# Kernel tuning notes

Hardware: AMD Instinct MI355X
Metric: run time of the kernel (lower is better)

The kernel has to match this reference:

```python
import jax, jax.numpy as jnp
import numpy as np

N, E, G = 50000, 640000, 1024
D, RD, H = 128, 200, 512
NUM_ATOM_FEATS, ATOM_VOCAB = 9, 64
NUM_BOND_FEATS, BOND_VOCAB = 3, 16


def setup_inputs() -> dict:
    key = jax.random.key(0)
    ks = jax.random.split(key, 24)
    inp = {
        "x_feat": jax.random.randint(ks[0], (N, NUM_ATOM_FEATS), 0, ATOM_VOCAB),
        "edge_index": jax.random.randint(ks[1], (2, E), 0, N),
        "edge_attr_feat": jax.random.randint(ks[2], (E, NUM_BOND_FEATS), 0, BOND_VOCAB),
        "batch": jnp.sort(jax.random.randint(ks[3], (N,), 0, G)),
        "rdkit_feats": jax.random.normal(ks[4], (G, RD), dtype=jnp.float32),
        # learned params
        "atom_emb": jax.random.normal(ks[5], (NUM_ATOM_FEATS, ATOM_VOCAB, D), dtype=jnp.float32) * 0.02,
        "bond_emb": jax.random.normal(ks[6], (NUM_BOND_FEATS, BOND_VOCAB, D), dtype=jnp.float32) * 0.02,
        "conv1_w1": jax.random.normal(ks[7], (D, D), dtype=jnp.float32) / np.sqrt(D),
        "conv1_b1": jnp.zeros((D,), jnp.float32),
        "conv1_w2": jax.random.normal(ks[8], (D, D), dtype=jnp.float32) / np.sqrt(D),
        "conv1_b2": jnp.zeros((D,), jnp.float32),
        "conv2_w1": jax.random.normal(ks[9], (D, D), dtype=jnp.float32) / np.sqrt(D),
        "conv2_b1": jnp.zeros((D,), jnp.float32),
        "conv2_w2": jax.random.normal(ks[10], (D, D), dtype=jnp.float32) / np.sqrt(D),
        "conv2_b2": jnp.zeros((D,), jnp.float32),
        "mlp_w1": jax.random.normal(ks[11], (D + RD, H), dtype=jnp.float32) / np.sqrt(D + RD),
        "mlp_b1": jnp.zeros((H,), jnp.float32),
        "mlp_w2": jax.random.normal(ks[12], (H, H // 2), dtype=jnp.float32) / np.sqrt(H),
        "mlp_b2": jnp.zeros((H // 2,), jnp.float32),
        "mlp_w3": jax.random.normal(ks[13], (H // 2, 1), dtype=jnp.float32) / np.sqrt(H // 2),
        "mlp_b3": jnp.zeros((1,), jnp.float32),
    }
    return inp


def _gine_conv(x, edge_index, edge_attr, w1, b1, w2, b2, eps=0.0):
    # PyG GINEConv: out = nn((1+eps)*x + sum_{j in N(i)} relu(x_j + e_ji))
    src, dst = edge_index[0], edge_index[1]
    msg = jax.nn.relu(x[src] + edge_attr)               # [E, D]
    agg = jax.ops.segment_sum(msg, dst, num_segments=x.shape[0])  # [N, D]
    h = (1.0 + eps) * x + agg
    h = jax.nn.relu(h @ w1 + b1)
    return h @ w2 + b2


def reference(x_feat, edge_index, edge_attr_feat, batch, rdkit_feats,
              atom_emb, bond_emb,
              conv1_w1, conv1_b1, conv1_w2, conv1_b2,
              conv2_w1, conv2_b1, conv2_w2, conv2_b2,
              mlp_w1, mlp_b1, mlp_w2, mlp_b2, mlp_w3, mlp_b3):
    # AtomEncoder / BondEncoder: sum of per-feature categorical embeddings
    x = atom_emb[jnp.arange(NUM_ATOM_FEATS)[None, :], x_feat].sum(axis=1)          # [N, D]
    edge_attr = bond_emb[jnp.arange(NUM_BOND_FEATS)[None, :], edge_attr_feat].sum(axis=1)  # [E, D]

    x = _gine_conv(x, edge_index, edge_attr, conv1_w1, conv1_b1, conv1_w2, conv1_b2)
    x = _gine_conv(x, edge_index, edge_attr, conv2_w1, conv2_b1, conv2_w2, conv2_b2)

    # global mean pool over graphs
    sums = jax.ops.segment_sum(x, batch, num_segments=G)                # [G, D]
    counts = jax.ops.segment_sum(jnp.ones((x.shape[0],), x.dtype), batch, num_segments=G)
    pooled = sums / jnp.maximum(counts, 1.0)[:, None]

    h = jnp.concatenate([pooled, rdkit_feats], axis=1)                  # [G, D+RD]
    h = jax.nn.relu(h @ mlp_w1 + mlp_b1)   # dropout is identity in eval mode
    h = jax.nn.relu(h @ mlp_w2 + mlp_b2)
    return h @ mlp_w3 + mlp_b3                                          # [G, 1]
```

## Files before the change

### kernel.cpp

```cpp
#include <hip/hip_runtime.h>

#define N_NODES 50000
#define N_EDGES 640000
#define N_GRAPH 1024
#define D 128
#define RD 200
#define CAP 64

typedef __attribute__((ext_vector_type(4))) float f32x4;
typedef __attribute__((ext_vector_type(8))) float f32x8;
typedef __attribute__((ext_vector_type(4))) _Float16 half4;
typedef __attribute__((ext_vector_type(8))) _Float16 half8;

__global__ void k_prep(const float* __restrict__ w0, const float* __restrict__ w1,
                       const float* __restrict__ w2, const float* __restrict__ w3,
                       const float* __restrict__ mw1, const float* __restrict__ mw2,
                       const float* __restrict__ emb,
                       _Float16* __restrict__ cWf,
                       _Float16* __restrict__ W1f,
                       _Float16* __restrict__ W2f,
                       _Float16* __restrict__ embh,
                       int* __restrict__ deg) {
  int t = blockIdx.x * 256 + threadIdx.x;
  if (t < N_NODES) deg[t] = 0;
  if (t < 8192) {
    int mat = t >> 11, r = t & 2047;
    int frag = r >> 6, lane = r & 63;
    int n0 = frag >> 2, kk = frag & 3;
    int n = n0 * 16 + (lane & 15);
    int kb = (lane >> 4) * 8 + kk * 32;
    const float* W = (mat == 0) ? w0 : (mat == 1) ? w1 : (mat == 2) ? w2 : w3;
    half8 o;
#pragma unroll
    for (int j = 0; j < 8; ++j) o[j] = (_Float16)W[(kb + j) * D + n];
    *(half8*)&cWf[((size_t)mat * 2048 + r) * 8] = o;
  } else if (t < 8192 + 22528) {
    int u = t - 8192;
    int frag = u >> 6, lane = u & 63;
    int n0 = frag / 11, kk = frag % 11;
    int n = n0 * 16 + (lane & 15);
    int kb = (lane >> 4) * 8 + kk * 32;
    half8 o;
#pragma unroll
    for (int j = 0; j < 8; ++j) {
      int k = kb + j;
      o[j] = (k < 328) ? (_Float16)mw1[k * 512 + n] : (_Float16)0.f;
    }
    *(half8*)&W1f[(size_t)u * 8] = o;
  } else if (t < 8192 + 22528 + 16384) {
    int u = t - 8192 - 22528;
    int frag = u >> 6, lane = u & 63;
    int n0 = frag >> 4, kk = frag & 15;
    int n = n0 * 16 + (lane & 15);
    int kb = (lane >> 4) * 8 + kk * 32;
    half8 o;
#pragma unroll
    for (int j = 0; j < 8; ++j) o[j] = (_Float16)mw2[(kb + j) * 256 + n];
    *(half8*)&W2f[(size_t)u * 8] = o;
  } else if (t < 8192 + 22528 + 16384 + 9216) {
    int u = t - 8192 - 22528 - 16384;
    float4 v0 = *(const float4*)&emb[(size_t)u * 8];
    float4 v1 = *(const float4*)&emb[(size_t)u * 8 + 4];
    half8 o;
    o[0] = (_Float16)v0.x; o[1] = (_Float16)v0.y; o[2] = (_Float16)v0.z; o[3] = (_Float16)v0.w;
    o[4] = (_Float16)v1.x; o[5] = (_Float16)v1.y; o[6] = (_Float16)v1.z; o[7] = (_Float16)v1.w;
    *(half8*)&embh[(size_t)u * 8] = o;
  }
}

__global__ void k_atom_count(const int* __restrict__ xf, const _Float16* __restrict__ embh,
                             _Float16* __restrict__ x16,
                             const int* __restrict__ ei, const int* __restrict__ bondf,
                             const int* __restrict__ batch,
                             int* __restrict__ deg, int* __restrict__ csr1,
                             int* __restrict__ gstart) {
  if (blockIdx.x < 3125) {
    int t = blockIdx.x * 256 + threadIdx.x;
    int node = t >> 4, c = (t & 15) << 3;
    if ((t & 15) == 0) {
      int b = batch[node];
      int prev = (node == 0) ? -1 : batch[node - 1];
      for (int g = prev + 1; g <= b; ++g) gstart[g] = node;
      if (node == N_NODES - 1)
        for (int g = b + 1; g <= N_GRAPH; ++g) gstart[g] = N_NODES;
    }
    int v[9];
#pragma unroll
    for (int f = 0; f < 9; ++f) v[f] = xf[node * 9 + f];
    f32x8 a = (f32x8)(0.f);
#pragma unroll
    for (int f = 0; f < 9; ++f) {
      half8 e8 = *(const half8*)&embh[(size_t)(f * 64 + v[f]) * D + c];
      a += __builtin_convertvector(e8, f32x8);
    }
    half8 o;
#pragma unroll
    for (int tt = 0; tt < 8; ++tt) o[tt] = (_Float16)a[tt];
    *(half8*)&x16[(size_t)node * D + c] = o;
  } else {
    int e = (blockIdx.x - 3125) * 256 + threadIdx.x;
    if (e < N_EDGES) {
      int d = ei[N_EDGES + e];
      int rank = atomicAdd(&deg[d], 1);
      int s = ei[e];
      int f0 = bondf[e * 3], f1 = bondf[e * 3 + 1], f2 = bondf[e * 3 + 2];
      if (rank < CAP)
        csr1[(d << 6) | rank] = s | (f0 << 16) | (f1 << 20) | (f2 << 24);
    }
  }
}

__global__ __launch_bounds__(256) void k_agg(
    const _Float16* __restrict__ X, const int* __restrict__ deg,
    const int* __restrict__ csr1, const float* __restrict__ bemb,
    _Float16* __restrict__ out) {
  __shared__ half8 sB[48 * 16];
  for (int t = threadIdx.x; t < 768; t += blockDim.x) {
    float4 v0 = *(const float4*)&bemb[t * 8];
    float4 v1 = *(const float4*)&bemb[t * 8 + 4];
    half8 h;
    h[0] = (_Float16)v0.x; h[1] = (_Float16)v0.y; h[2] = (_Float16)v0.z; h[3] = (_Float16)v0.w;
    h[4] = (_Float16)v1.x; h[5] = (_Float16)v1.y; h[6] = (_Float16)v1.z; h[7] = (_Float16)v1.w;
    sB[t] = h;
  }
  __syncthreads();
  int lane = threadIdx.x & 63;
  int quad = lane >> 4, l15 = lane & 15, c8 = l15 * 8;
  int wid = blockIdx.x * 4 + (threadIdx.x >> 6);
  int nw = gridDim.x * 4;
  for (int i = wid; i < N_NODES; i += nw) {
    int degn = deg[i];
    int dq = degn > CAP ? CAP : degn;
    int e0 = i << 6;
    int creg = (lane < dq) ? csr1[e0 + lane] : 0;
    f32x8 ac0 = (f32x8)(0.f), ac1 = (f32x8)(0.f);
    for (int jb = 0; jb < dq; jb += 8) {
      unsigned e0v = (unsigned)__shfl(creg, jb + quad);
      unsigned e1v = (unsigned)__shfl(creg, jb + 4 + quad);
      if (jb + quad < dq) {
        half8 x0 = *(const half8*)&X[(size_t)(e0v & 0xFFFF) * D + c8];
        unsigned p0 = e0v >> 16;
        half8 m0h = (x0 + sB[(p0 & 15) * 16 + l15]) +
                    (sB[256 + ((p0 >> 4) & 15) * 16 + l15] + sB[512 + (p0 >> 8) * 16 + l15]);
        f32x8 g0 = __builtin_convertvector(m0h, f32x8);
#pragma unroll
        for (int tt = 0; tt < 8; ++tt) ac0[tt] += fmaxf(g0[tt], 0.f);
      }
      if (jb + 4 + quad < dq) {
        half8 x1 = *(const half8*)&X[(size_t)(e1v & 0xFFFF) * D + c8];
        unsigned p1 = e1v >> 16;
        half8 m1h = (x1 + sB[(p1 & 15) * 16 + l15]) +
                    (sB[256 + ((p1 >> 4) & 15) * 16 + l15] + sB[512 + (p1 >> 8) * 16 + l15]);
        f32x8 g1 = __builtin_convertvector(m1h, f32x8);
#pragma unroll
        for (int tt = 0; tt < 8; ++tt) ac1[tt] += fmaxf(g1[tt], 0.f);
      }
    }
    f32x8 acc = ac0 + ac1;
#pragma unroll
    for (int tt = 0; tt < 8; ++tt) {
      acc[tt] += __shfl_xor(acc[tt], 16);
      acc[tt] += __shfl_xor(acc[tt], 32);
    }
    if (quad == 0) {
      half8 sr = *(const half8*)&X[(size_t)i * D + c8];
      f32x8 o = __builtin_convertvector(sr, f32x8) + acc;
      half8 oh;
#pragma unroll
      for (int tt = 0; tt < 8; ++tt) oh[tt] = (_Float16)o[tt];
      *(half8*)&out[(size_t)i * D + c8] = oh;
    }
  }
}

__global__ __launch_bounds__(256) void k_conv(
    const _Float16* __restrict__ A,
    const _Float16* __restrict__ W1f, const float* __restrict__ b1,
    const _Float16* __restrict__ W2f, const float* __restrict__ b2,
    _Float16* __restrict__ O16) {
  __shared__ _Float16 sW[2048 * 8];
  __shared__ _Float16 sI[128 * 136];
  int tid = threadIdx.x, w = tid >> 6, lane = tid & 63;
  int m0 = blockIdx.x * 128;
  int col16 = lane & 15, q = lane >> 4;
  for (int t = tid; t < 2048; t += 256)
    *(float4*)&sW[t * 8] = *(const float4*)&W1f[(size_t)t * 8];
  half8 afr[2][4];
#pragma unroll
  for (int f = 0; f < 2; ++f) {
    int row = m0 + w * 32 + f * 16 + col16;
    if (row >= N_NODES) row = N_NODES - 1;
    const _Float16* Ar = A + (size_t)row * D + q * 8;
#pragma unroll
    for (int kk = 0; kk < 4; ++kk) afr[f][kk] = *(const half8*)(Ar + kk * 32);
  }
  __syncthreads();
#pragma unroll
  for (int n0 = 0; n0 < 8; ++n0) {
    f32x4 a0 = {0.f, 0.f, 0.f, 0.f}, a1 = {0.f, 0.f, 0.f, 0.f};
#pragma unroll
    for (int kk = 0; kk < 4; ++kk) {
      half8 b = *(const half8*)&sW[((n0 * 4 + kk) * 64 + lane) * 8];
      a0 = __builtin_amdgcn_mfma_f32_16x16x32_f16(afr[0][kk], b, a0, 0, 0, 0);
      a1 = __builtin_amdgcn_mfma_f32_16x16x32_f16(afr[1][kk], b, a1, 0, 0, 0);
    }
    float bb = b1[n0 * 16 + col16];
#pragma unroll
    for (int r = 0; r < 4; ++r) {
      sI[(w * 32 + q * 4 + r) * 136 + n0 * 16 + col16] = (_Float16)fmaxf(a0[r] + bb, 0.f);
      sI[(w * 32 + 16 + q * 4 + r) * 136 + n0 * 16 + col16] = (_Float16)fmaxf(a1[r] + bb, 0.f);
    }
  }
  __syncthreads();
  for (int t = tid; t < 2048; t += 256)
    *(float4*)&sW[t * 8] = *(const float4*)&W2f[(size_t)t * 8];
  half8 a2[2][4];
#pragma unroll
  for (int f = 0; f < 2; ++f) {
    const _Float16* tr = &sI[(w * 32 + f * 16 + col16) * 136 + q * 8];
#pragma unroll
    for (int kk = 0; kk < 4; ++kk) a2[f][kk] = *(const half8*)(tr + kk * 32);
  }
  __syncthreads();
#pragma unroll
  for (int n0 = 0; n0 < 8; ++n0) {
    f32x4 a0 = {0.f, 0.f, 0.f, 0.f}, a1 = {0.f, 0.f, 0.f, 0.f};
#pragma unroll
    for (int kk = 0; kk < 4; ++kk) {
      half8 b = *(const half8*)&sW[((n0 * 4 + kk) * 64 + lane) * 8];
      a0 = __builtin_amdgcn_mfma_f32_16x16x32_f16(a2[0][kk], b, a0, 0, 0, 0);
      a1 = __builtin_amdgcn_mfma_f32_16x16x32_f16(a2[1][kk], b, a1, 0, 0, 0);
    }
    int col = n0 * 16 + col16;
    float bb = b2[col];
#pragma unroll
    for (int r = 0; r < 4; ++r) {
      int r0 = m0 + w * 32 + q * 4 + r;
      int r1 = r0 + 16;
      if (r0 < N_NODES) O16[(size_t)r0 * D + col] = (_Float16)(a0[r] + bb);
      if (r1 < N_NODES) O16[(size_t)r1 * D + col] = (_Float16)(a1[r] + bb);
    }
  }
}

__global__ __launch_bounds__(256) void k_pool(
    const _Float16* __restrict__ x, const int* __restrict__ gstart,
    const float* __restrict__ rdkit, _Float16* __restrict__ hcat,
    const float* __restrict__ B3, float* __restrict__ out) {
  int g = blockIdx.x * 4 + (threadIdx.x >> 6);
  if (g >= N_GRAPH) return;
  int lane = threadIdx.x & 63;
  int half_ = lane >> 5;
  int c4 = (lane & 31) * 4;
  int lo = gstart[g];
  int hi = gstart[g + 1];
  f32x4 a = {0.f, 0.f, 0.f, 0.f};
  for (int i = lo + half_; i < hi; i += 2) {
    half4 v = *(const half4*)&x[(size_t)i * D + c4];
    a += __builtin_convertvector(v, f32x4);
  }
#pragma unroll
  for (int t = 0; t < 4; ++t) a[t] += __shfl_xor(a[t], 32);
  float inv = 1.f / fmaxf((float)(hi - lo), 1.f);
  if (half_ == 0) {
    half4 o;
    o.x = (_Float16)(a[0] * inv); o.y = (_Float16)(a[1] * inv);
    o.z = (_Float16)(a[2] * inv); o.w = (_Float16)(a[3] * inv);
    *(half4*)&hcat[(size_t)g * 352 + c4] = o;
  }
  for (int r = lane; r < RD; r += 64)
    hcat[(size_t)g * 352 + D + r] = (_Float16)rdkit[(size_t)g * RD + r];
  if (lane < 24) hcat[(size_t)g * 352 + 328 + lane] = (_Float16)0.f;
  if (lane == 0) out[g] = B3[0];
}

__global__ __launch_bounds__(256) void k_mlp1(
    const _Float16* __restrict__ A, const _Float16* __restrict__ W1f,
    const float* __restrict__ B, _Float16* __restrict__ O) {
  int w = threadIdx.x >> 6, lane = threadIdx.x & 63;
  int gid = blockIdx.x * 4 + w;
  int mt = gid >> 5, n0 = gid & 31;
  int col16 = lane & 15, q = lane >> 4;
  const _Float16* Ar = A + (size_t)(mt * 16 + col16) * 352 + q * 8;
  f32x4 acc = {0.f, 0.f, 0.f, 0.f};
#pragma unroll
  for (int kk = 0; kk < 11; ++kk) {
    half8 a = *(const half8*)(Ar + kk * 32);
    half8 b = *(const half8*)&W1f[(size_t)((n0 * 11 + kk) * 64 + lane) * 8];
    acc = __builtin_amdgcn_mfma_f32_16x16x32_f16(a, b, acc, 0, 0, 0);
  }
  int col = n0 * 16 + col16;
  float bb = B[col];
#pragma unroll
  for (int r = 0; r < 4; ++r) {
    int row = mt * 16 + q * 4 + r;
    O[(size_t)row * 512 + col] = (_Float16)fmaxf(acc[r] + bb, 0.f);
  }
}

__global__ __launch_bounds__(256) void k_mlp23(
    const _Float16* __restrict__ A, const _Float16* __restrict__ W2f,
    const float* __restrict__ B2, const float* __restrict__ W3,
    float* __restrict__ out) {
  int w = threadIdx.x >> 6, lane = threadIdx.x & 63;
  int gid = blockIdx.x * 4 + w;
  int mt = gid >> 4, n0 = gid & 15;
  int col16 = lane & 15, q = lane >> 4;
  const _Float16* Ar = A + (size_t)(mt * 16 + col16) * 512 + q * 8;
  f32x4 acc = {0.f, 0.f, 0.f, 0.f};
#pragma unroll
  for (int kk = 0; kk < 16; ++kk) {
    half8 a = *(const half8*)(Ar + kk * 32);
    half8 b = *(const half8*)&W2f[(size_t)((n0 * 16 + kk) * 64 + lane) * 8];
    acc = __builtin_amdgcn_mfma_f32_16x16x32_f16(a, b, acc, 0, 0, 0);
  }
  int col = n0 * 16 + col16;
  float bb = B2[col], w3 = W3[col];
  float p[4];
#pragma unroll
  for (int r = 0; r < 4; ++r) p[r] = fmaxf(acc[r] + bb, 0.f) * w3;
#pragma unroll
  for (int r = 0; r < 4; ++r) {
    p[r] += __shfl_xor(p[r], 1);
    p[r] += __shfl_xor(p[r], 2);
    p[r] += __shfl_xor(p[r], 4);
    p[r] += __shfl_xor(p[r], 8);
  }
  if (col16 == 0) {
#pragma unroll
    for (int r = 0; r < 4; ++r)
      atomicAdd(&out[mt * 16 + q * 4 + r], p[r]);
  }
}

extern "C" void kernel_launch(void* const* d_in, const int* in_sizes, int n_in,
                              void* d_out, int out_size, void* d_ws, size_t ws_size,
                              hipStream_t stream) {
  const int* x_feat = (const int*)d_in[0];
  const int* ei = (const int*)d_in[1];
  const int* bondf = (const int*)d_in[2];
  const int* batch = (const int*)d_in[3];
  const float* rdkit = (const float*)d_in[4];
  const float* atom_emb = (const float*)d_in[5];
  const float* bond_emb = (const float*)d_in[6];
  const float* c1w1 = (const float*)d_in[7];
  const float* c1b1 = (const float*)d_in[8];
  const float* c1w2 = (const float*)d_in[9];
  const float* c1b2 = (const float*)d_in[10];
  const float* c2w1 = (const float*)d_in[11];
  const float* c2b1 = (const float*)d_in[12];
  const float* c2w2 = (const float*)d_in[13];
  const float* c2b2 = (const float*)d_in[14];
  const float* mw1 = (const float*)d_in[15];
  const float* mb1 = (const float*)d_in[16];
  const float* mw2 = (const float*)d_in[17];
  const float* mb2 = (const float*)d_in[18];
  const float* mw3 = (const float*)d_in[19];
  const float* mb3 = (const float*)d_in[20];
  float* out = (float*)d_out;

  char* ws = (char*)d_ws;
  size_t off = 0;
  auto alloc = [&](size_t bytes) {
    void* p = ws + off;
    off += (bytes + 255) & ~(size_t)255;
    return p;
  };
  _Float16* x16a = (_Float16*)alloc((size_t)N_NODES * D * 2);
  _Float16* x16b = (_Float16*)alloc((size_t)N_NODES * D * 2);
  _Float16* h16 = (_Float16*)alloc((size_t)N_NODES * D * 2);
  _Float16* x2_16 = (_Float16*)alloc((size_t)N_NODES * D * 2);
  int* deg = (int*)alloc((size_t)N_NODES * 4);
  int* csr1 = (int*)alloc((size_t)N_NODES * CAP * 4);
  int* gstart = (int*)alloc((size_t)(N_GRAPH + 1) * 4);
  _Float16* hcat16 = (_Float16*)alloc((size_t)N_GRAPH * 352 * 2);
  _Float16* h1buf = (_Float16*)alloc((size_t)N_GRAPH * 512 * 2);
  _Float16* cWf = (_Float16*)alloc((size_t)4 * 2048 * 8 * 2);
  _Float16* W1f = (_Float16*)alloc((size_t)352 * 64 * 8 * 2);
  _Float16* W2f = (_Float16*)alloc((size_t)256 * 64 * 8 * 2);
  _Float16* embh = (_Float16*)alloc((size_t)9 * 64 * D * 2);

  k_prep<<<256, 256, 0, stream>>>(c1w1, c1w2, c2w1, c2w2, mw1, mw2, atom_emb,
                                  cWf, W1f, W2f, embh, deg);
  k_atom_count<<<3125 + 2500, 256, 0, stream>>>(x_feat, embh, x16a,
                                                ei, bondf, batch,
                                                deg, csr1, gstart);

  int ctiles = (N_NODES + 127) / 128;
  k_agg<<<2048, 256, 0, stream>>>(x16a, deg, csr1, bond_emb, h16);
  k_conv<<<ctiles, 256, 0, stream>>>(h16, cWf + 0 * 16384, c1b1,
                                     cWf + 1 * 16384, c1b2, x16b);
  k_agg<<<2048, 256, 0, stream>>>(x16b, deg, csr1, bond_emb, h16);
  k_conv<<<ctiles, 256, 0, stream>>>(h16, cWf + 2 * 16384, c2b1,
                                     cWf + 3 * 16384, c2b2, x2_16);

  k_pool<<<N_GRAPH / 4, 256, 0, stream>>>(x2_16, gstart, rdkit, hcat16, mb3, out);
  k_mlp1<<<512, 256, 0, stream>>>(hcat16, W1f, mb1, h1buf);
  k_mlp23<<<256, 256, 0, stream>>>(h1buf, W2f, mb2, mw3, out);

  (void)in_sizes; (void)n_in; (void)out_size; (void)ws_size;
}
```

Baseline: 277.0 us.

## Split CSR fill into separate pass, prefetch agg rows, fuse MLP layers

```diff
diff --git a/kernel.cpp b/kernel.cpp
--- a/kernel.cpp
+++ b/kernel.cpp
@@ -72,7 +72,7 @@
                              _Float16* __restrict__ x16,
                              const int* __restrict__ ei, const int* __restrict__ bondf,
                              const int* __restrict__ batch,
-                             int* __restrict__ deg, int* __restrict__ csr1,
+                             int* __restrict__ deg, int2* __restrict__ drep,
                              int* __restrict__ gstart) {
   if (blockIdx.x < 3125) {
     int t = blockIdx.x * 256 + threadIdx.x;
@@ -104,10 +104,18 @@
       int rank = atomicAdd(&deg[d], 1);
       int s = ei[e];
       int f0 = bondf[e * 3], f1 = bondf[e * 3 + 1], f2 = bondf[e * 3 + 2];
-      if (rank < CAP)
-        csr1[(d << 6) | rank] = s | (f0 << 16) | (f1 << 20) | (f2 << 24);
-    }
-  }
+      drep[e] = make_int2(d | (rank << 16), s | (f0 << 16) | (f1 << 20) | (f2 << 24));
+    }
+  }
+}
+
+__global__ void k_fill(const int2* __restrict__ drep, int* __restrict__ csr1) {
+  int e = blockIdx.x * 256 + threadIdx.x;
+  if (e >= N_EDGES) return;
+  int2 v = drep[e];
+  int d = v.x & 0xFFFF;
+  int rank = ((unsigned)v.x) >> 16;
+  if (rank < CAP) csr1[(d << 6) | rank] = v.y;
 }
 
 __global__ __launch_bounds__(256) void k_agg(
@@ -128,11 +136,16 @@
   int quad = lane >> 4, l15 = lane & 15, c8 = l15 * 8;
   int wid = blockIdx.x * 4 + (threadIdx.x >> 6);
   int nw = gridDim.x * 4;
+  if (wid >= N_NODES) return;
+  int pdeg = deg[wid];
+  int pcreg = csr1[(wid << 6) + lane];
   for (int i = wid; i < N_NODES; i += nw) {
-    int degn = deg[i];
+    int degn = pdeg;
+    int creg = pcreg;
+    int i2 = (i + nw < N_NODES) ? i + nw : i;
+    pdeg = deg[i2];
+    pcreg = csr1[(i2 << 6) + lane];
     int dq = degn > CAP ? CAP : degn;
-    int e0 = i << 6;
-    int creg = (lane < dq) ? csr1[e0 + lane] : 0;
     f32x8 ac0 = (f32x8)(0.f), ac1 = (f32x8)(0.f);
     for (int jb = 0; jb < dq; jb += 8) {
       unsigned e0v = (unsigned)__shfl(creg, jb + quad);
@@ -274,62 +287,69 @@
   if (lane == 0) out[g] = B3[0];
 }
 
-__global__ __launch_bounds__(256) void k_mlp1(
+__global__ __launch_bounds__(512) void k_mlp(
     const _Float16* __restrict__ A, const _Float16* __restrict__ W1f,
-    const float* __restrict__ B, _Float16* __restrict__ O) {
-  int w = threadIdx.x >> 6, lane = threadIdx.x & 63;
-  int gid = blockIdx.x * 4 + w;
-  int mt = gid >> 5, n0 = gid & 31;
-  int col16 = lane & 15, q = lane >> 4;
-  const _Float16* Ar = A + (size_t)(mt * 16 + col16) * 352 + q * 8;
-  f32x4 acc = {0.f, 0.f, 0.f, 0.f};
-#pragma unroll
-  for (int kk = 0; kk < 11; ++kk) {
-    half8 a = *(const half8*)(Ar + kk * 32);
-    half8 b = *(const half8*)&W1f[(size_t)((n0 * 11 + kk) * 64 + lane) * 8];
-    acc = __builtin_amdgcn_mfma_f32_16x16x32_f16(a, b, acc, 0, 0, 0);
-  }
-  int col = n0 * 16 + col16;
-  float bb = B[col];
-#pragma unroll
-  for (int r = 0; r < 4; ++r) {
-    int row = mt * 16 + q * 4 + r;
-    O[(size_t)row * 512 + col] = (_Float16)fmaxf(acc[r] + bb, 0.f);
-  }
-}
-
-__global__ __launch_bounds__(256) void k_mlp23(
-    const _Float16* __restrict__ A, const _Float16* __restrict__ W2f,
+    const float* __restrict__ B1, const _Float16* __restrict__ W2f,
     const float* __restrict__ B2, const float* __restrict__ W3,
     float* __restrict__ out) {
-  int w = threadIdx.x >> 6, lane = threadIdx.x & 63;
-  int gid = blockIdx.x * 4 + w;
-  int mt = gid >> 4, n0 = gid & 15;
+  __shared__ _Float16 sH1[16 * 520];
+  int tid = threadIdx.x, w = tid >> 6, lane = tid & 63;
+  int mt = blockIdx.x;
   int col16 = lane & 15, q = lane >> 4;
-  const _Float16* Ar = A + (size_t)(mt * 16 + col16) * 512 + q * 8;
-  f32x4 acc = {0.f, 0.f, 0.f, 0.f};
-#pragma unroll
-  for (int kk = 0; kk < 16; ++kk) {
-    half8 a = *(const half8*)(Ar + kk * 32);
-    half8 b = *(const half8*)&W2f[(size_t)((n0 * 16 + kk) * 64 + lane) * 8];
-    acc = __builtin_amdgcn_mfma_f32_16x16x32_f16(a, b, acc, 0, 0, 0);
-  }
-  int col = n0 * 16 + col16;
-  float bb = B2[col], w3 = W3[col];
-  float p[4];
-#pragma unroll
-  for (int r = 0; r < 4; ++r) p[r] = fmaxf(acc[r] + bb, 0.f) * w3;
-#pragma unroll
-  for (int r = 0; r < 4; ++r) {
-    p[r] += __shfl_xor(p[r], 1);
-    p[r] += __shfl_xor(p[r], 2);
-    p[r] += __shfl_xor(p[r], 4);
-    p[r] += __shfl_xor(p[r], 8);
-  }
-  if (col16 == 0) {
-#pragma unroll
-    for (int r = 0; r < 4; ++r)
-      atomicAdd(&out[mt * 16 + q * 4 + r], p[r]);
+  {
+    half8 afr[11];
+    const _Float16* Ar = A + (size_t)(mt * 16 + col16) * 352 + q * 8;
+#pragma unroll
+    for (int kk = 0; kk < 11; ++kk) afr[kk] = *(const half8*)(Ar + kk * 32);
+#pragma unroll
+    for (int ng = 0; ng < 4; ++ng) {
+      int n0 = w * 4 + ng;
+      f32x4 acc = {0.f, 0.f, 0.f, 0.f};
+#pragma unroll
+      for (int kk = 0; kk < 11; ++kk) {
+        half8 b = *(const half8*)&W1f[(size_t)((n0 * 11 + kk) * 64 + lane) * 8];
+        acc = __builtin_amdgcn_mfma_f32_16x16x32_f16(afr[kk], b, acc, 0, 0, 0);
+      }
+      int col = n0 * 16 + col16;
+      float bb = B1[col];
+#pragma unroll
+      for (int r = 0; r < 4; ++r)
+        sH1[(q * 4 + r) * 520 + col] = (_Float16)fmaxf(acc[r] + bb, 0.f);
+    }
+  }
+  __syncthreads();
+  {
+    half8 a2[16];
+    const _Float16* Ar = &sH1[col16 * 520 + q * 8];
+#pragma unroll
+    for (int kk = 0; kk < 16; ++kk) a2[kk] = *(const half8*)(Ar + kk * 32);
+    float p[4] = {0.f, 0.f, 0.f, 0.f};
+#pragma unroll
+    for (int ng = 0; ng < 2; ++ng) {
+      int n0 = w * 2 + ng;
+      f32x4 acc = {0.f, 0.f, 0.f, 0.f};
+#pragma unroll
+      for (int kk = 0; kk < 16; ++kk) {
+        half8 b = *(const half8*)&W2f[(size_t)((n0 * 16 + kk) * 64 + lane) * 8];
+        acc = __builtin_amdgcn_mfma_f32_16x16x32_f16(a2[kk], b, acc, 0, 0, 0);
+      }
+      int col = n0 * 16 + col16;
+      float bb = B2[col], w3 = W3[col];
+#pragma unroll
+      for (int r = 0; r < 4; ++r) p[r] += fmaxf(acc[r] + bb, 0.f) * w3;
+    }
+#pragma unroll
+    for (int r = 0; r < 4; ++r) {
+      p[r] += __shfl_xor(p[r], 1);
+      p[r] += __shfl_xor(p[r], 2);
+      p[r] += __shfl_xor(p[r], 4);
+      p[r] += __shfl_xor(p[r], 8);
+    }
+    if (col16 == 0) {
+#pragma unroll
+      for (int r = 0; r < 4; ++r)
+        atomicAdd(&out[mt * 16 + q * 4 + r], p[r]);
+    }
   }
 }
 
@@ -372,9 +392,9 @@
   _Float16* x2_16 = (_Float16*)alloc((size_t)N_NODES * D * 2);
   int* deg = (int*)alloc((size_t)N_NODES * 4);
   int* csr1 = (int*)alloc((size_t)N_NODES * CAP * 4);
+  int2* drep = (int2*)alloc((size_t)N_EDGES * 8);
   int* gstart = (int*)alloc((size_t)(N_GRAPH + 1) * 4);
   _Float16* hcat16 = (_Float16*)alloc((size_t)N_GRAPH * 352 * 2);
-  _Float16* h1buf = (_Float16*)alloc((size_t)N_GRAPH * 512 * 2);
   _Float16* cWf = (_Float16*)alloc((size_t)4 * 2048 * 8 * 2);
   _Float16* W1f = (_Float16*)alloc((size_t)352 * 64 * 8 * 2);
   _Float16* W2f = (_Float16*)alloc((size_t)256 * 64 * 8 * 2);
@@ -384,7 +404,8 @@
                                   cWf, W1f, W2f, embh, deg);
   k_atom_count<<<3125 + 2500, 256, 0, stream>>>(x_feat, embh, x16a,
                                                 ei, bondf, batch,
-                                                deg, csr1, gstart);
+                                                deg, drep, gstart);
+  k_fill<<<(N_EDGES + 255) / 256, 256, 0, stream>>>(drep, csr1);
 
   int ctiles = (N_NODES + 127) / 128;
   k_agg<<<2048, 256, 0, stream>>>(x16a, deg, csr1, bond_emb, h16);
@@ -395,8 +416,7 @@
                                      cWf + 3 * 16384, c2b2, x2_16);
 
   k_pool<<<N_GRAPH / 4, 256, 0, stream>>>(x2_16, gstart, rdkit, hcat16, mb3, out);
-  k_mlp1<<<512, 256, 0, stream>>>(hcat16, W1f, mb1, h1buf);
-  k_mlp23<<<256, 256, 0, stream>>>(h1buf, W2f, mb2, mw3, out);
+  k_mlp<<<N_GRAPH / 16, 512, 0, stream>>>(hcat16, W1f, mb1, W2f, mb2, mw3, out);
 
   (void)in_sizes; (void)n_in; (void)out_size; (void)ws_size;
 }
```

Result: faster. 266.1 us (-3.9%).
